# Kernel optimization log

Hardware: AMD Instinct MI355X
Metric: run time of the kernel (lower is better)

The kernel has to match this reference:

```python
import jax, jax.numpy as jnp
import numpy as np

INPUTDIM = 256
OUTDIM = 256
GRIDSIZE = 300
SCALE_BASE = 1.0
SCALE_FOURIER = 1.0
BATCH = 2048


def setup_inputs() -> dict:
    key = jax.random.key(0)
    k_x, k_bw, k_fc = jax.random.split(key, 3)
    x = jax.random.normal(k_x, (BATCH, INPUTDIM), dtype=jnp.float32)
    # HeUniform for base_weight: limit = sqrt(6 / fan_in)
    limit = np.sqrt(6.0 / INPUTDIM)
    base_weight = jax.random.uniform(
        k_bw, (INPUTDIM, OUTDIM), dtype=jnp.float32, minval=-limit, maxval=limit)
    stddev = 1.0 / (np.sqrt(INPUTDIM) * np.sqrt(GRIDSIZE))
    fouriercoeffs = (jax.random.normal(k_fc, (2, OUTDIM, INPUTDIM, GRIDSIZE), dtype=jnp.float32)
                     * jnp.float32(stddev))
    return {"x": x, "base_weight": base_weight, "fouriercoeffs": fouriercoeffs}


def reference(x, base_weight, fouriercoeffs):
    # Base path: silu(x @ W)
    base_output = jax.nn.silu(x @ base_weight)  # [B, J]
    # Fourier feature expansion: k = 1..gridsize
    k = jnp.arange(1, GRIDSIZE + 1, dtype=x.dtype)  # [K]
    theta = x[:, :, None] * k[None, None, :]        # [B, I, K]
    c = jnp.cos(theta)
    s = jnp.sin(theta)
    # einsum 'dbik,djik->bj' split into cos and sin parts
    fourier_output = (jnp.einsum('bik,jik->bj', c, fouriercoeffs[0])
                      + jnp.einsum('bik,jik->bj', s, fouriercoeffs[1]))
    return SCALE_BASE * base_output + SCALE_FOURIER * fourier_output
```

## Files before the change

### kernel.cpp

```cpp
#include <hip/hip_runtime.h>
#include <hip/hip_bf16.h>
#include <cstdint>

#define BATCH   2048
#define INDIM   256
#define OUTDIM  256
#define KGRID   300
#define NCHUNK  10

typedef __attribute__((ext_vector_type(4))) float f32x4;
typedef __attribute__((ext_vector_type(2))) float f32x2;
typedef __attribute__((ext_vector_type(8))) short bf16x8;

__device__ __forceinline__ uint32_t pack_bf16x2(float lo, float hi) {
    union { __hip_bfloat162 h; uint32_t u; } cv;
    cv.h = __float22bfloat162_rn(make_float2(lo, hi));
    return cv.u;
}

__device__ __forceinline__ f32x2 pk_fma_sub(f32x2 a, f32x2 b, f32x2 c) {
    f32x2 d;
    asm("v_pk_fma_f32 %0, %1, %2, %3 neg_lo:[0,0,1] neg_hi:[0,0,1]"
        : "=v"(d) : "v"(a), "v"(b), "v"(c));
    return d;
}

__device__ __forceinline__ void load_lds16(const void* g, void* l) {
    __builtin_amdgcn_global_load_lds(
        (const __attribute__((address_space(1))) void*)g,
        (__attribute__((address_space(3))) void*)l, 16, 0, 0);
}

__device__ __forceinline__ bf16x8 zero_frag() {
    union { uint32_t u[4]; bf16x8 v; } z = {{0u, 0u, 0u, 0u}};
    return z.v;
}

__device__ __forceinline__ bf16x8 gen_frag(float ck, float sk,
                                           float c1, float s1) {
    float cp = __builtin_fmaf(ck, c1,  sk * s1);
    float sp = __builtin_fmaf(sk, c1, -ck * s1);
    f32x2 C; C.x = ck; C.y = sk;
    f32x2 P; P.x = cp; P.y = sp;
    f32x2 T2; T2.x = c1 + c1; T2.y = c1 + c1;
    union { uint32_t u[4]; bf16x8 v; } r;
    #pragma unroll
    for (int q = 0; q < 4; ++q) {
        r.u[q] = pack_bf16x2(C.x, C.y);
        f32x2 N = pk_fma_sub(T2, C, P);
        P = C; C = N;
    }
    return r.v;
}

#define PACKED_U4 ((size_t)INDIM * NCHUNK * OUTDIM * 8)
#define PACKED_BYTES (PACKED_U4 * 16)

__global__ __launch_bounds__(256) void pack_kernel(
    const float* __restrict__ fc, uint4* __restrict__ pk)
{
    size_t tidg = (size_t)blockIdx.x * 256 + threadIdx.x;
    int sub = tidg & 7;
    int j   = (tidg >> 3) & 255;
    int ich = (int)(tidg >> 11);
    int ch  = ich % NCHUNK;
    int i   = ich / NCHUNK;
    int kb  = ch * 32 + (sub ^ (j & 7)) * 4;
    if (kb > KGRID - 4) kb = KGRID - 4;
    const float* pc = fc + ((size_t)j * INDIM + i) * KGRID + kb;
    const float* ps = pc + (size_t)OUTDIM * INDIM * KGRID;
    float4 vc = *reinterpret_cast<const float4*>(pc);
    float4 vs = *reinterpret_cast<const float4*>(ps);
    uint4 wv;
    wv.x = pack_bf16x2(vc.x, vs.x);
    wv.y = pack_bf16x2(vc.y, vs.y);
    wv.z = pack_bf16x2(vc.z, vs.z);
    wv.w = pack_bf16x2(vc.w, vs.w);
    pk[tidg] = wv;
}

__global__ __launch_bounds__(256, 2) void fourier_dma_kernel(
    const float* __restrict__ x, const uint4* __restrict__ pk,
    float* __restrict__ part)
{
    __shared__ uint4 Bbuf[2][256][8];

    const int tid = threadIdx.x;
    const int flat = blockIdx.x + (blockIdx.z << 4);
    const int L  = (flat & 7) * 64 + (flat >> 3);
    const int b0 = (L & 15) * 128;
    const int z  = L >> 4;
    const int i0 = z * 8;

    const int lane = tid & 63, wave = tid >> 6;
    const int wrow = wave * 32;
    const int lrow = lane & 15, lgrp = lane >> 4;
    const int q8 = wave * 8;

    f32x4 acc[2][16] = {};

    float thn[2];
    float c1[2], s1[2];
    float c16[2], s16[2];
    float cS[2], sS[2];

    #pragma unroll
    for (int mf = 0; mf < 2; ++mf)
        thn[mf] = x[(size_t)(b0 + wrow + mf * 16 + lrow) * INDIM + i0];

    {
        const uint4* src = pk + (size_t)(i0 * NCHUNK) * 2048;
        char* dst = (char*)&Bbuf[0][0][0];
        #pragma unroll
        for (int q = 0; q < 8; ++q)
            load_lds16(src + (q8 + q) * 64 + lane, dst + (q8 + q) * 1024);
    }

    int il = 0, ch = 0;
    #pragma unroll 1
    for (int t = 0; t < 8 * NCHUNK; ++t) {
        __syncthreads();
        {
            int il2 = il, ch2 = ch + 1;
            if (ch2 == NCHUNK) { ch2 = 0; il2 = (il + 1 < 8) ? il + 1 : il; }
            const uint4* src = pk + (size_t)((i0 + il2) * NCHUNK + ch2) * 2048;
            char* dst = (char*)&Bbuf[(t + 1) & 1][0][0];
            #pragma unroll
            for (int q = 0; q < 8; ++q)
                load_lds16(src + (q8 + q) * 64 + lane, dst + (q8 + q) * 1024);
        }
        if (ch == 0) {
            const float flg = (float)(lgrp * 4);
            #pragma unroll
            for (int mf = 0; mf < 2; ++mf) {
                float th = thn[mf];
                __sincosf(th, &s1[mf], &c1[mf]);
                __sincosf(16.f * th, &s16[mf], &c16[mf]);
                float a0 = __builtin_fmaf(flg, th, th);
                __sincosf(a0, &sS[mf], &cS[mf]);
            }
            int iln = (il + 1 < 8) ? il + 1 : il;
            #pragma unroll
            for (int mf = 0; mf < 2; ++mf)
                thn[mf] = x[(size_t)(b0 + wrow + mf * 16 + lrow) * INDIM
                            + i0 + iln];
        }
        bf16x8 af[2][2];
        #pragma unroll
        for (int mf = 0; mf < 2; ++mf) {
            af[0][mf] = gen_frag(cS[mf], sS[mf], c1[mf], s1[mf]);
            float ck = __builtin_fmaf(cS[mf], c16[mf], -sS[mf] * s16[mf]);
            float sk = __builtin_fmaf(sS[mf], c16[mf],  cS[mf] * s16[mf]);
            af[1][mf] = gen_frag(ck, sk, c1[mf], s1[mf]);
            cS[mf] = __builtin_fmaf(ck, c16[mf], -sk * s16[mf]);
            sS[mf] = __builtin_fmaf(sk, c16[mf],  ck * s16[mf]);
        }
        if (ch == NCHUNK - 1) {
            #pragma unroll
            for (int mf = 0; mf < 2; ++mf) {
                af[0][mf] = (lgrp == 3) ? zero_frag() : af[0][mf];
                af[1][mf] = zero_frag();
            }
        }
        __builtin_amdgcn_s_setprio(1);
        #pragma unroll
        for (int s = 0; s < 2; ++s) {
            const int swz = (s * 4 + lgrp) ^ (lrow & 7);
            #pragma unroll
            for (int g = 0; g < 4; ++g) {
                bf16x8 bfr[4];
                #pragma unroll
                for (int q = 0; q < 4; ++q) {
                    const int jl = (g * 4 + q) * 16 + lrow;
                    uint4 tv = Bbuf[t & 1][jl][swz];
                    bfr[q] = *reinterpret_cast<bf16x8*>(&tv);
                }
                #pragma unroll
                for (int mf = 0; mf < 2; ++mf)
                    #pragma unroll
                    for (int q = 0; q < 4; ++q)
                        acc[mf][g * 4 + q] = __builtin_amdgcn_mfma_f32_16x16x32_bf16(
                            af[s][mf], bfr[q], acc[mf][g * 4 + q], 0, 0, 0);
            }
        }
        __builtin_amdgcn_s_setprio(0);
        if (++ch == NCHUNK) { ch = 0; ++il; }
    }

    float* pws = part + (size_t)z * BATCH * OUTDIM;
    #pragma unroll
    for (int mf = 0; mf < 2; ++mf)
        #pragma unroll
        for (int nf = 0; nf < 16; ++nf)
            #pragma unroll
            for (int r = 0; r < 4; ++r) {
                int b = b0 + wrow + mf * 16 + lgrp * 4 + r;
                int j = nf * 16 + lrow;
                pws[(size_t)b * OUTDIM + j] = acc[mf][nf][r];
            }
}

__global__ __launch_bounds__(256, 2) void fourier_kernel_fb(
    const float* __restrict__ x, const float* __restrict__ fc,
    float* __restrict__ ws, int ips)
{
    __shared__ uint4 Abuf[2][128][8];
    __shared__ uint4 Bbuf[128][8];

    const int tid  = threadIdx.x;
    const int b0   = blockIdx.x * 256;
    const int j0   = blockIdx.y * 128;
    const int i0   = blockIdx.z * ips;

    const int lane = tid & 63, wave = tid >> 6;
    const int wm   = wave >> 1, wn = wave & 1;
    const int lrow = lane & 15, lgrp = lane >> 4;
    const int grow = tid >> 1,  gh = tid & 1;

    f32x4 acc[2][4][4] = {};

    #pragma unroll 1
    for (int il = 0; il < ips; ++il) {
        const int i = i0 + il;
        float th[2], c1[2], s1[2], t2[2];
        th[0] = x[(size_t)(b0 + grow)       * INDIM + i];
        th[1] = x[(size_t)(b0 + 128 + grow) * INDIM + i];
        #pragma unroll
        for (int m = 0; m < 2; ++m) {
            __sincosf(th[m], &s1[m], &c1[m]);
            t2[m] = 2.f * c1[m];
        }
        #pragma unroll 1
        for (int ch = 0; ch < NCHUNK; ++ch) {
            #pragma unroll
            for (int r = 0; r < 4; ++r) {
                int flat = r * 256 + tid;
                int jl = flat >> 3, sub = flat & 7;
                int kb = ch * 32 + sub * 4;
                if (kb > KGRID - 4) kb = KGRID - 4;
                const float* pc = fc + ((size_t)(j0 + jl) * INDIM + i) * KGRID + kb;
                const float* ps = pc + (size_t)OUTDIM * INDIM * KGRID;
                float4 vc = *reinterpret_cast<const float4*>(pc);
                float4 vs = *reinterpret_cast<const float4*>(ps);
                uint4 wv;
                wv.x = pack_bf16x2(vc.x, vs.x);
                wv.y = pack_bf16x2(vc.y, vs.y);
                wv.z = pack_bf16x2(vc.z, vs.z);
                wv.w = pack_bf16x2(vc.w, vs.w);
                Bbuf[jl][sub ^ (jl & 7)] = wv;
            }
            #pragma unroll
            for (int m = 0; m < 2; ++m) {
                const int k0 = ch * 32 + gh * 16;
                float ck, sk;
                __sincosf(th[m] * (float)(k0 + 1), &sk, &ck);
                float cp = __builtin_fmaf(ck, c1[m],  sk * s1[m]);
                float sp = __builtin_fmaf(sk, c1[m], -ck * s1[m]);
                const int swz = grow & 7;
                #pragma unroll
                for (int c = 0; c < 4; ++c) {
                    uint32_t uu[4];
                    #pragma unroll
                    for (int qq = 0; qq < 4; ++qq) {
                        const int kidx = k0 + c * 4 + qq;
                        float cc = (kidx < KGRID) ? ck : 0.f;
                        float ss = (kidx < KGRID) ? sk : 0.f;
                        uu[qq] = pack_bf16x2(cc, ss);
                        float cn = __builtin_fmaf(t2[m], ck, -cp);
                        float sn = __builtin_fmaf(t2[m], sk, -sp);
                        cp = ck; sp = sk; ck = cn; sk = sn;
                    }
                    Abuf[m][grow][(gh * 4 + c) ^ swz] =
                        make_uint4(uu[0], uu[1], uu[2], uu[3]);
                }
            }
            __syncthreads();
            #pragma unroll
            for (int s = 0; s < 2; ++s) {
                bf16x8 bfr[4];
                #pragma unroll
                for (int nf = 0; nf < 4; ++nf) {
                    const int jl = wn * 64 + nf * 16 + lrow;
                    uint4 tv = Bbuf[jl][(s * 4 + lgrp) ^ (jl & 7)];
                    bfr[nf] = *reinterpret_cast<bf16x8*>(&tv);
                }
                #pragma unroll
                for (int m = 0; m < 2; ++m) {
                    #pragma unroll
                    for (int mf = 0; mf < 4; ++mf) {
                        const int rowA = wm * 64 + mf * 16 + lrow;
                        uint4 tv = Abuf[m][rowA][(s * 4 + lgrp) ^ (rowA & 7)];
                        bf16x8 af = *reinterpret_cast<bf16x8*>(&tv);
                        #pragma unroll
                        for (int nf = 0; nf < 4; ++nf)
                            acc[m][mf][nf] = __builtin_amdgcn_mfma_f32_16x16x32_bf16(
                                af, bfr[nf], acc[m][mf][nf], 0, 0, 0);
                    }
                }
            }
            __syncthreads();
        }
    }

    float* pws = ws + (size_t)blockIdx.z * BATCH * OUTDIM;
    #pragma unroll
    for (int m = 0; m < 2; ++m)
        #pragma unroll
        for (int mf = 0; mf < 4; ++mf)
            #pragma unroll
            for (int nf = 0; nf < 4; ++nf)
                #pragma unroll
                for (int r = 0; r < 4; ++r) {
                    int b = b0 + m * 128 + wm * 64 + mf * 16 + lgrp * 4 + r;
                    int j = j0 + wn * 64 + nf * 16 + lrow;
                    pws[(size_t)b * OUTDIM + j] = acc[m][mf][nf][r];
                }
}

__global__ __launch_bounds__(256) void combine_kernel(
    const float* __restrict__ x, const float* __restrict__ w,
    const float* __restrict__ part, float* __restrict__ out, int nsplit)
{
    __shared__ float Xs[64][16];
    __shared__ float Wt[16][68];

    const int tid = threadIdx.x;
    const int b0 = blockIdx.x * 64;
    const int j0 = blockIdx.y * 64;
    const int tx = tid & 15, ty = tid >> 4;

    float acc[4][4] = {};

    for (int kb = 0; kb < INDIM; kb += 16) {
        {
            int m = tid >> 2, kq = (tid & 3) * 4;
            float4 v = *reinterpret_cast<const float4*>(
                &x[(size_t)(b0 + m) * INDIM + kb + kq]);
            Xs[m][kq+0] = v.x; Xs[m][kq+1] = v.y; Xs[m][kq+2] = v.z; Xs[m][kq+3] = v.w;
        }
        {
            int kr = tid >> 4, jc = (tid & 15) * 4;
            float4 v = *reinterpret_cast<const float4*>(
                &w[(size_t)(kb + kr) * OUTDIM + j0 + jc]);
            Wt[kr][jc+0] = v.x; Wt[kr][jc+1] = v.y; Wt[kr][jc+2] = v.z; Wt[kr][jc+3] = v.w;
        }
        __syncthreads();
        #pragma unroll
        for (int kk = 0; kk < 16; ++kk) {
            float a[4], b[4];
            #pragma unroll
            for (int q = 0; q < 4; ++q) { a[q] = Xs[ty*4+q][kk]; b[q] = Wt[kk][tx*4+q]; }
            #pragma unroll
            for (int q = 0; q < 4; ++q)
                #pragma unroll
                for (int p = 0; p < 4; ++p)
                    acc[q][p] = __builtin_fmaf(a[q], b[p], acc[q][p]);
        }
        __syncthreads();
    }

    float psum[4][4] = {};
    for (int s = 0; s < nsplit; ++s) {
        const float* base = part + (size_t)s * BATCH * OUTDIM;
        #pragma unroll
        for (int q = 0; q < 4; ++q) {
            float4 pv = *reinterpret_cast<const float4*>(
                &base[(size_t)(b0 + ty*4 + q) * OUTDIM + j0 + tx*4]);
            psum[q][0] += pv.x; psum[q][1] += pv.y;
            psum[q][2] += pv.z; psum[q][3] += pv.w;
        }
    }

    #pragma unroll
    for (int q = 0; q < 4; ++q)
        #pragma unroll
        for (int p = 0; p < 4; ++p) {
            float v = acc[q][p];
            float sv = v / (1.f + __expf(-v));
            out[(size_t)(b0 + ty*4 + q) * OUTDIM + (j0 + tx*4 + p)] =
                sv + psum[q][p];
        }
}

extern "C" void kernel_launch(void* const* d_in, const int* in_sizes, int n_in,
                              void* d_out, int out_size, void* d_ws, size_t ws_size,
                              hipStream_t stream) {
    const float* x  = (const float*)d_in[0];
    const float* bw = (const float*)d_in[1];
    const float* fc = (const float*)d_in[2];
    float* out = (float*)d_out;

    const size_t per = (size_t)BATCH * OUTDIM * sizeof(float);

    if (ws_size >= PACKED_BYTES + 32 * per) {
        uint4* pk   = (uint4*)d_ws;
        float* part = (float*)((char*)d_ws + PACKED_BYTES);
        pack_kernel<<<(int)(PACKED_U4 / 256), 256, 0, stream>>>(fc, pk);
        fourier_dma_kernel<<<dim3(16, 1, 32), 256, 0, stream>>>(x, pk, part);
        combine_kernel<<<dim3(BATCH / 64, OUTDIM / 64), 256, 0, stream>>>(
            x, bw, part, out, 32);
    } else {
        float* part = (float*)d_ws;
        int S = 32;
        while (S > 1 && (size_t)S * per > ws_size) S >>= 1;
        const int ips = INDIM / S;
        fourier_kernel_fb<<<dim3(BATCH / 256, OUTDIM / 128, S), 256, 0, stream>>>(
            x, fc, part, ips);
        combine_kernel<<<dim3(BATCH / 64, OUTDIM / 64), 256, 0, stream>>>(
            x, bw, part, out, S);
    }
}
```

Before: 224.9 us.

## Split B tile between LDS and direct register loads; store partials as bf16

The packed Fourier coefficients are split so the first 192 output columns go through the LDS double buffer, while the last 64 columns are packed in MFMA fragment order and loaded straight from global memory into registers on each step. This shrinks LDS traffic and the footprint per block, and may let more blocks fit. Split-K partial sums are now written and read as bf16 rather than fp32, halving partial-buffer traffic between the Fourier and combine kernels. The cost is lower precision when the 32 partials are summed, plus extra global load latency inside the MFMA loop.

Result: slower. 249.2 us (+10.8%).

```diff
diff --git a/kernel.cpp b/kernel.cpp
--- a/kernel.cpp
+++ b/kernel.cpp
@@ -7,6 +7,7 @@
 #define OUTDIM  256
 #define KGRID   300
 #define NCHUNK  10
+#define JLDS    192
 
 typedef __attribute__((ext_vector_type(4))) float f32x4;
 typedef __attribute__((ext_vector_type(2))) float f32x2;
@@ -16,6 +17,10 @@
     union { __hip_bfloat162 h; uint32_t u; } cv;
     cv.h = __float22bfloat162_rn(make_float2(lo, hi));
     return cv.u;
+}
+
+__device__ __forceinline__ float bfu2f(unsigned short u) {
+    union { unsigned short s[2]; float f; } c; c.s[0] = 0; c.s[1] = u; return c.f;
 }
 
 __device__ __forceinline__ f32x2 pk_fma_sub(f32x2 a, f32x2 b, f32x2 c) {
@@ -53,37 +58,68 @@
     return r.v;
 }
 
-#define PACKED_U4 ((size_t)INDIM * NCHUNK * OUTDIM * 8)
-#define PACKED_BYTES (PACKED_U4 * 16)
+#define PKL_U4 ((size_t)INDIM * NCHUNK * JLDS * 8)
+#define PKH_U4 ((size_t)INDIM * NCHUNK * 2 * 4 * 64)
+#define PKL_BYTES (PKL_U4 * 16)
+#define PKH_BYTES (PKH_U4 * 16)
+#define PART_BYTES ((size_t)32 * BATCH * OUTDIM * 2)
 
 __global__ __launch_bounds__(256) void pack_kernel(
-    const float* __restrict__ fc, uint4* __restrict__ pk)
+    const float* __restrict__ fc, uint4* __restrict__ pkl,
+    uint4* __restrict__ pkh)
 {
     size_t tidg = (size_t)blockIdx.x * 256 + threadIdx.x;
-    int sub = tidg & 7;
-    int j   = (tidg >> 3) & 255;
-    int ich = (int)(tidg >> 11);
-    int ch  = ich % NCHUNK;
-    int i   = ich / NCHUNK;
-    int kb  = ch * 32 + (sub ^ (j & 7)) * 4;
-    if (kb > KGRID - 4) kb = KGRID - 4;
-    const float* pc = fc + ((size_t)j * INDIM + i) * KGRID + kb;
-    const float* ps = pc + (size_t)OUTDIM * INDIM * KGRID;
-    float4 vc = *reinterpret_cast<const float4*>(pc);
-    float4 vs = *reinterpret_cast<const float4*>(ps);
-    uint4 wv;
-    wv.x = pack_bf16x2(vc.x, vs.x);
-    wv.y = pack_bf16x2(vc.y, vs.y);
-    wv.z = pack_bf16x2(vc.z, vs.z);
-    wv.w = pack_bf16x2(vc.w, vs.w);
-    pk[tidg] = wv;
+    int j, kb; uint4* dst;
+    if (tidg < PKL_U4) {
+        int sub = (int)(tidg & 7);
+        size_t rem = tidg >> 3;
+        j = (int)(rem % JLDS);
+        int ich = (int)(rem / JLDS);
+        int ch = ich % NCHUNK;
+        kb = ch * 32 + (sub ^ (j & 7)) * 4;
+        dst = pkl + tidg;
+        int i = ich / NCHUNK;
+        if (kb > KGRID - 4) kb = KGRID - 4;
+        const float* pc = fc + ((size_t)j * INDIM + i) * KGRID + kb;
+        const float* ps = pc + (size_t)OUTDIM * INDIM * KGRID;
+        float4 vc = *reinterpret_cast<const float4*>(pc);
+        float4 vs = *reinterpret_cast<const float4*>(ps);
+        uint4 wv;
+        wv.x = pack_bf16x2(vc.x, vs.x);
+        wv.y = pack_bf16x2(vc.y, vs.y);
+        wv.z = pack_bf16x2(vc.z, vs.z);
+        wv.w = pack_bf16x2(vc.w, vs.w);
+        *dst = wv;
+    } else {
+        size_t e = tidg - PKL_U4;
+        int lane = (int)(e & 63);
+        size_t rem = e >> 6;
+        int jb = (int)(rem & 3);
+        int s  = (int)((rem >> 2) & 1);
+        int ich = (int)(rem >> 3);
+        int ch = ich % NCHUNK;
+        int i  = ich / NCHUNK;
+        j = JLDS + jb * 16 + (lane & 15);
+        kb = ch * 32 + s * 16 + (lane >> 4) * 4;
+        if (kb > KGRID - 4) kb = KGRID - 4;
+        const float* pc = fc + ((size_t)j * INDIM + i) * KGRID + kb;
+        const float* ps = pc + (size_t)OUTDIM * INDIM * KGRID;
+        float4 vc = *reinterpret_cast<const float4*>(pc);
+        float4 vs = *reinterpret_cast<const float4*>(ps);
+        uint4 wv;
+        wv.x = pack_bf16x2(vc.x, vs.x);
+        wv.y = pack_bf16x2(vc.y, vs.y);
+        wv.z = pack_bf16x2(vc.z, vs.z);
+        wv.w = pack_bf16x2(vc.w, vs.w);
+        pkh[e] = wv;
+    }
 }
 
 __global__ __launch_bounds__(256, 2) void fourier_dma_kernel(
-    const float* __restrict__ x, const uint4* __restrict__ pk,
-    float* __restrict__ part)
+    const float* __restrict__ x, const uint4* __restrict__ pkl,
+    const uint4* __restrict__ pkh, __hip_bfloat16* __restrict__ part)
 {
-    __shared__ uint4 Bbuf[2][256][8];
+    __shared__ uint4 Bbuf[2][JLDS][8];
 
     const int tid = threadIdx.x;
     const int flat = blockIdx.x + (blockIdx.z << 4);
@@ -95,7 +131,7 @@
     const int lane = tid & 63, wave = tid >> 6;
     const int wrow = wave * 32;
     const int lrow = lane & 15, lgrp = lane >> 4;
-    const int q8 = wave * 8;
+    const int q6 = wave * 6;
 
     f32x4 acc[2][16] = {};
 
@@ -109,25 +145,31 @@
         thn[mf] = x[(size_t)(b0 + wrow + mf * 16 + lrow) * INDIM + i0];
 
     {
-        const uint4* src = pk + (size_t)(i0 * NCHUNK) * 2048;
+        const uint4* src = pkl + (size_t)(i0 * NCHUNK) * (JLDS * 8);
         char* dst = (char*)&Bbuf[0][0][0];
         #pragma unroll
-        for (int q = 0; q < 8; ++q)
-            load_lds16(src + (q8 + q) * 64 + lane, dst + (q8 + q) * 1024);
+        for (int q = 0; q < 6; ++q)
+            load_lds16(src + (q6 + q) * 64 + lane, dst + (q6 + q) * 1024);
     }
 
     int il = 0, ch = 0;
     #pragma unroll 1
     for (int t = 0; t < 8 * NCHUNK; ++t) {
         __syncthreads();
+        const uint4* hsrc = pkh + ((size_t)(i0 + il) * NCHUNK + ch) * 512;
+        uint4 h0 = hsrc[lane];
+        uint4 h1 = hsrc[64 + lane];
+        uint4 h2 = hsrc[128 + lane];
+        uint4 h3 = hsrc[192 + lane];
         {
             int il2 = il, ch2 = ch + 1;
             if (ch2 == NCHUNK) { ch2 = 0; il2 = (il + 1 < 8) ? il + 1 : il; }
-            const uint4* src = pk + (size_t)((i0 + il2) * NCHUNK + ch2) * 2048;
+            const uint4* src =
+                pkl + (size_t)((i0 + il2) * NCHUNK + ch2) * (JLDS * 8);
             char* dst = (char*)&Bbuf[(t + 1) & 1][0][0];
             #pragma unroll
-            for (int q = 0; q < 8; ++q)
-                load_lds16(src + (q8 + q) * 64 + lane, dst + (q8 + q) * 1024);
+            for (int q = 0; q < 6; ++q)
+                load_lds16(src + (q6 + q) * 64 + lane, dst + (q6 + q) * 1024);
         }
         if (ch == 0) {
             const float flg = (float)(lgrp * 4);
@@ -167,7 +209,7 @@
         for (int s = 0; s < 2; ++s) {
             const int swz = (s * 4 + lgrp) ^ (lrow & 7);
             #pragma unroll
-            for (int g = 0; g < 4; ++g) {
+            for (int g = 0; g < 3; ++g) {
                 bf16x8 bfr[4];
                 #pragma unroll
                 for (int q = 0; q < 4; ++q) {
@@ -182,12 +224,35 @@
                         acc[mf][g * 4 + q] = __builtin_amdgcn_mfma_f32_16x16x32_bf16(
                             af[s][mf], bfr[q], acc[mf][g * 4 + q], 0, 0, 0);
             }
+            {
+                bf16x8 bh0 = *reinterpret_cast<bf16x8*>(&h0);
+                bf16x8 bh1 = *reinterpret_cast<bf16x8*>(&h1);
+                bf16x8 bh2 = *reinterpret_cast<bf16x8*>(&h2);
+                bf16x8 bh3 = *reinterpret_cast<bf16x8*>(&h3);
+                #pragma unroll
+                for (int mf = 0; mf < 2; ++mf) {
+                    acc[mf][12] = __builtin_amdgcn_mfma_f32_16x16x32_bf16(
+                        af[s][mf], bh0, acc[mf][12], 0, 0, 0);
+                    acc[mf][13] = __builtin_amdgcn_mfma_f32_16x16x32_bf16(
+                        af[s][mf], bh1, acc[mf][13], 0, 0, 0);
+                    acc[mf][14] = __builtin_amdgcn_mfma_f32_16x16x32_bf16(
+                        af[s][mf], bh2, acc[mf][14], 0, 0, 0);
+                    acc[mf][15] = __builtin_amdgcn_mfma_f32_16x16x32_bf16(
+                        af[s][mf], bh3, acc[mf][15], 0, 0, 0);
+                }
+            }
+            if (s == 0) {
+                h0 = hsrc[256 + lane];
+                h1 = hsrc[320 + lane];
+                h2 = hsrc[384 + lane];
+                h3 = hsrc[448 + lane];
+            }
         }
         __builtin_amdgcn_s_setprio(0);
         if (++ch == NCHUNK) { ch = 0; ++il; }
     }
 
-    float* pws = part + (size_t)z * BATCH * OUTDIM;
+    __hip_bfloat16* pws = part + (size_t)z * BATCH * OUTDIM;
     #pragma unroll
     for (int mf = 0; mf < 2; ++mf)
         #pragma unroll
@@ -196,13 +261,13 @@
             for (int r = 0; r < 4; ++r) {
                 int b = b0 + wrow + mf * 16 + lgrp * 4 + r;
                 int j = nf * 16 + lrow;
-                pws[(size_t)b * OUTDIM + j] = acc[mf][nf][r];
+                pws[(size_t)b * OUTDIM + j] = __float2bfloat16(acc[mf][nf][r]);
             }
 }
 
 __global__ __launch_bounds__(256, 2) void fourier_kernel_fb(
     const float* __restrict__ x, const float* __restrict__ fc,
-    float* __restrict__ ws, int ips)
+    __hip_bfloat16* __restrict__ ws, int ips)
 {
     __shared__ uint4 Abuf[2][128][8];
     __shared__ uint4 Bbuf[128][8];
@@ -302,7 +367,7 @@
         }
     }
 
-    float* pws = ws + (size_t)blockIdx.z * BATCH * OUTDIM;
+    __hip_bfloat16* pws = ws + (size_t)blockIdx.z * BATCH * OUTDIM;
     #pragma unroll
     for (int m = 0; m < 2; ++m)
         #pragma unroll
@@ -313,13 +378,15 @@
                 for (int r = 0; r < 4; ++r) {
                     int b = b0 + m * 128 + wm * 64 + mf * 16 + lgrp * 4 + r;
                     int j = j0 + wn * 64 + nf * 16 + lrow;
-                    pws[(size_t)b * OUTDIM + j] = acc[m][mf][nf][r];
+                    pws[(size_t)b * OUTDIM + j] =
+                        __float2bfloat16(acc[m][mf][nf][r]);
                 }
 }
 
 __global__ __launch_bounds__(256) void combine_kernel(
     const float* __restrict__ x, const float* __restrict__ w,
-    const float* __restrict__ part, float* __restrict__ out, int nsplit)
+    const __hip_bfloat16* __restrict__ part, float* __restrict__ out,
+    int nsplit)
 {
     __shared__ float Xs[64][16];
     __shared__ float Wt[16][68];
@@ -361,13 +428,13 @@
 
     float psum[4][4] = {};
     for (int s = 0; s < nsplit; ++s) {
-        const float* base = part + (size_t)s * BATCH * OUTDIM;
+        const __hip_bfloat16* base = part + (size_t)s * BATCH * OUTDIM;
         #pragma unroll
         for (int q = 0; q < 4; ++q) {
-            float4 pv = *reinterpret_cast<const float4*>(
+            ushort4 pv = *reinterpret_cast<const ushort4*>(
                 &base[(size_t)(b0 + ty*4 + q) * OUTDIM + j0 + tx*4]);
-            psum[q][0] += pv.x; psum[q][1] += pv.y;
-            psum[q][2] += pv.z; psum[q][3] += pv.w;
+            psum[q][0] += bfu2f(pv.x); psum[q][1] += bfu2f(pv.y);
+            psum[q][2] += bfu2f(pv.z); psum[q][3] += bfu2f(pv.w);
         }
     }
 
@@ -390,17 +457,21 @@
     const float* fc = (const float*)d_in[2];
     float* out = (float*)d_out;
 
-    const size_t per = (size_t)BATCH * OUTDIM * sizeof(float);
-
-    if (ws_size >= PACKED_BYTES + 32 * per) {
-        uint4* pk   = (uint4*)d_ws;
-        float* part = (float*)((char*)d_ws + PACKED_BYTES);
-        pack_kernel<<<(int)(PACKED_U4 / 256), 256, 0, stream>>>(fc, pk);
-        fourier_dma_kernel<<<dim3(16, 1, 32), 256, 0, stream>>>(x, pk, part);
+    const size_t per = (size_t)BATCH * OUTDIM * 2;
+
+    if (ws_size >= PKL_BYTES + PKH_BYTES + PART_BYTES) {
+        uint4* pkl = (uint4*)d_ws;
+        uint4* pkh = (uint4*)((char*)d_ws + PKL_BYTES);
+        __hip_bfloat16* part =
+            (__hip_bfloat16*)((char*)d_ws + PKL_BYTES + PKH_BYTES);
+        pack_kernel<<<(int)((PKL_U4 + PKH_U4) / 256), 256, 0, stream>>>(
+            fc, pkl, pkh);
+        fourier_dma_kernel<<<dim3(16, 1, 32), 256, 0, stream>>>(
+            x, pkl, pkh, part);
         combine_kernel<<<dim3(BATCH / 64, OUTDIM / 64), 256, 0, stream>>>(
             x, bw, part, out, 32);
     } else {
-        float* part = (float*)d_ws;
+        __hip_bfloat16* part = (__hip_bfloat16*)d_ws;
         int S = 32;
         while (S > 1 && (size_t)S * per > ws_size) S >>= 1;
         const int ips = INDIM / S;
```
